# Optimization experiments

Hardware: AMD Instinct MI355X
Metric: run time of the kernel (lower is better)

The kernel has to match this reference:

```python
import jax, jax.numpy as jnp
import numpy as np

N_CLASS = 50257
EMB = 1024
HID = 1024
BATCH = 1024  # must equal HID due to the module's [H,H] zero state init
SEQ = 128


def setup_inputs() -> dict:
    key = jax.random.key(0)
    ks = jax.random.split(key, 8)
    s_e = 1.0 / np.sqrt(EMB)
    s_h = 1.0 / np.sqrt(HID)
    X = jax.random.randint(ks[0], (BATCH, SEQ), 0, N_CLASS, dtype=jnp.int32)
    C = jax.random.normal(ks[1], (N_CLASS, EMB), dtype=jnp.float32)
    # gate order along last axis: i, f, g, o (each block of size HID)
    Wx = jax.random.uniform(ks[2], (EMB, 4 * HID), jnp.float32, -s_e, s_e)
    bx = jax.random.uniform(ks[3], (4 * HID,), jnp.float32, -s_e, s_e)
    Wh = jax.random.uniform(ks[4], (HID, 4 * HID), jnp.float32, -s_h, s_h)
    bh = jax.random.uniform(ks[5], (4 * HID,), jnp.float32, -s_h, s_h)
    W_out = jax.random.uniform(ks[6], (HID, N_CLASS), jnp.float32, -s_h, s_h)
    b_out = jnp.ones((N_CLASS,), dtype=jnp.float32)  # nn.Parameter(torch.ones)
    return {"X": X, "C": C, "Wx": Wx, "bx": bx, "Wh": Wh, "bh": bh,
            "W_out": W_out, "b_out": b_out}


def _lstm_last_hidden(xs, Wx, bx, Wh, bh):
    # xs: [S, B, E]; with zero-initialized h/c of shape [H,H] and B == H,
    # the original broadcast-buggy code reduces to a standard LSTM.
    x_proj = jnp.einsum('sbe,eg->sbg', xs, Wx) + bx  # [S, B, 4H]
    B = xs.shape[1]
    H = Wh.shape[0]
    h0 = jnp.zeros((B, H), dtype=xs.dtype)
    c0 = jnp.zeros((B, H), dtype=xs.dtype)

    def step(carry, xp):
        h, c = carry
        gates = xp + h @ Wh + bh  # [B, 4H]
        i, f, g, o = jnp.split(gates, 4, axis=-1)
        i = jax.nn.sigmoid(i)
        f = jax.nn.sigmoid(f)
        g = jnp.tanh(g)
        o = jax.nn.sigmoid(o)
        c = f * c + i * g
        h = o * jnp.tanh(c)
        return (h, c), None

    (h, _), _ = jax.lax.scan(step, (h0, c0), x_proj)
    return h  # [B, H] last timestep hidden


def reference(X, C, Wx, bx, Wh, bh, W_out, b_out):
    emb = C[X]                      # [B, S, E]
    xs = jnp.swapaxes(emb, 0, 1)    # [S, B, E]  (transpose(0,1))
    h_last = _lstm_last_hidden(xs, Wx, bx, Wh, bh)
    return h_last @ W_out + b_out   # [B, n_class]
```

## Files before the change

### kernel.cpp

```cpp
#include <hip/hip_runtime.h>
#include <hip/hip_bf16.h>

#define SEQ_   128
#define NCLS_  50257
#define EMB_   1024
#define HID_   1024
#define BATCH_ 1024
#define G4_    4096

typedef __attribute__((ext_vector_type(8))) short short8;
typedef __attribute__((ext_vector_type(4))) float f32x4;

__device__ __forceinline__ void async_copy16(void* lds, const void* g) {
  __builtin_amdgcn_global_load_lds(
      (const __attribute__((address_space(1))) void*)g,
      (__attribute__((address_space(3))) void*)lds, 16, 0, 0);
}

#define MFMA_ACC(c, a, b) \
  (c) = __builtin_amdgcn_mfma_f32_16x16x32_bf16((a), (b), (c), 0, 0, 0)

#define CFENCE() asm volatile("" ::: "memory")

__device__ __forceinline__ float sigmoidf_(float x) {
  return 1.f / (1.f + __expf(-x));
}
__device__ __forceinline__ float tanhf_(float x) {
  x = fminf(12.f, fmaxf(-12.f, x));
  float e = __expf(2.f * x);
  return (e - 1.f) / (e + 1.f);
}
__device__ __forceinline__ float bf2f_(ushort u) {
  return __uint_as_float(((unsigned int)u) << 16);
}

template <int EPI>
__global__ __launch_bounds__(256) void gemm_bt(
    const __hip_bfloat16* __restrict__ A, const __hip_bfloat16* __restrict__ Bt,
    float* __restrict__ outF, __hip_bfloat16* __restrict__ outB,
    int Mreal, int Nreal, int K, long ostride,
    const float* __restrict__ bias0) {
  __shared__ __align__(16) char smem[65536];

  const int tid = threadIdx.x;
  const int lane = tid & 63;
  const int w = tid >> 6;
  const int wm = w >> 1;
  const int wn = w & 1;
  const int m0 = blockIdx.y * 128;
  const int n0 = blockIdx.x * 128;

  const int fr = lane & 15;
  const int kb = (lane >> 4) * 16;
  const int swz = (fr & 7) << 4;

  f32x4 acc[4][4];
#pragma unroll
  for (int i = 0; i < 4; ++i)
#pragma unroll
    for (int j = 0; j < 4; ++j) acc[i][j] = (f32x4)(0.0f);

  auto STAGE = [&](int kc, int b) {
#pragma unroll
    for (int q = 0; q < 8; ++q) {
      const int ridx = (q & 3) * 256 + tid;
      const int row = ridx >> 3;
      const int ch = ridx & 7;
      const __hip_bfloat16* src;
      char* dst;
      if (q < 4) {
        long ar = m0 + row; if (ar >= Mreal) ar = Mreal - 1;
        src = A + ar * (long)K + kc * 64 + ch * 8;
        dst = smem + b * 16384 + ridx * 16;
      } else {
        long br = n0 + row; if (br >= Nreal) br = Nreal - 1;
        src = Bt + br * (long)K + kc * 64 + ch * 8;
        dst = smem + 32768 + b * 16384 + ridx * 16;
      }
      async_copy16(dst, src);
    }
  };

  const int KC = K >> 6;
  STAGE(0, 0);
  for (int kc = 0; kc < KC; ++kc) {
    const int b = kc & 1;
    if (kc + 1 < KC) {
      STAGE(kc + 1, b ^ 1);
      asm volatile("s_waitcnt vmcnt(8)" ::: "memory");
    } else {
      asm volatile("s_waitcnt vmcnt(0)" ::: "memory");
    }
    __builtin_amdgcn_s_barrier();
    CFENCE();

    short8 aR[2][4], bR[2][4];
#pragma unroll
    for (int kk = 0; kk < 2; ++kk)
#pragma unroll
      for (int f = 0; f < 4; ++f) {
        aR[kk][f] = *(const short8*)(smem + b * 16384 +
                     (wm * 64 + f * 16 + fr) * 128 + ((kk * 64 + kb) ^ swz));
        bR[kk][f] = *(const short8*)(smem + 32768 + b * 16384 +
                     (wn * 64 + f * 16 + fr) * 128 + ((kk * 64 + kb) ^ swz));
      }
#pragma unroll
    for (int fm = 0; fm < 4; ++fm)
#pragma unroll
      for (int fn = 0; fn < 4; ++fn) {
        MFMA_ACC(acc[fm][fn], aR[0][fm], bR[0][fn]);
        MFMA_ACC(acc[fm][fn], aR[1][fm], bR[1][fn]);
      }
    CFENCE();
    __builtin_amdgcn_s_barrier();
  }

  const int cn = lane & 15;
  const int rb = (lane >> 4) * 4;

  if (EPI == 0) {
    __hip_bfloat16* ldsC = (__hip_bfloat16*)smem;
#pragma unroll
    for (int fn = 0; fn < 4; ++fn) {
      const int col = wn * 64 + fn * 16 + cn;
      const float badd = bias0[n0 + col];
#pragma unroll
      for (int fm = 0; fm < 4; ++fm)
#pragma unroll
        for (int r = 0; r < 4; ++r)
          ldsC[(wm * 64 + fm * 16 + rb + r) * 136 + col] =
              __float2bfloat16(acc[fm][fn][r] + badd);
    }
    __syncthreads();
#pragma unroll
    for (int q = 0; q < 8; ++q) {
      const int chunk = q * 256 + tid;
      const int row = chunk >> 4;
      const int c8 = (chunk & 15) * 8;
      if (m0 + row < Mreal)
        *(short8*)(outB + (long)(m0 + row) * ostride + n0 + c8) =
            *(const short8*)(ldsC + row * 136 + c8);
    }
  } else {
    float* ldsC = (float*)smem;
#pragma unroll
    for (int half = 0; half < 2; ++half) {
      __syncthreads();
      if (wm == half) {
#pragma unroll
        for (int fn = 0; fn < 4; ++fn) {
          const int col = wn * 64 + fn * 16 + cn;
          const int gc = n0 + col;
          const float badd = (gc < Nreal) ? bias0[gc] : 0.f;
#pragma unroll
          for (int fm = 0; fm < 4; ++fm)
#pragma unroll
            for (int r = 0; r < 4; ++r)
              ldsC[(fm * 16 + rb + r) * 132 + col] = acc[fm][fn][r] + badd;
        }
      }
      __syncthreads();
#pragma unroll
      for (int it = 0; it < 32; ++it) {
        const int idx = it * 256 + tid;
        const int row = idx >> 7;
        const int col = idx & 127;
        const int grow = m0 + half * 64 + row;
        const int gcol = n0 + col;
        if (grow < Mreal && gcol < Nreal)
          outF[(long)grow * ostride + gcol] = ldsC[row * 132 + col];
      }
    }
  }
}

__global__ __launch_bounds__(256) void pack_b(const float* __restrict__ Wh,
                                              __hip_bfloat16* __restrict__ Bpk) {
  const int gtid = blockIdx.x * 256 + threadIdx.x;
  const int l = gtid & 63;
  const int tile = gtid >> 6;
  const int g = tile & 3;
  const int kk = (tile >> 2) & 1;
  const int kc = (tile >> 3) & 7;
  const int kh = (tile >> 6) & 1;
  const int wn = (tile >> 7) & 1;
  const int ht = tile >> 8;
  const int h = ht * 32 + wn * 16 + (l & 15);
  const int k0 = kh * 512 + kc * 64 + kk * 32 + (l >> 4) * 8;
  short8 v;
#pragma unroll
  for (int e = 0; e < 8; ++e) {
    const __hip_bfloat16 b = __float2bfloat16(Wh[(size_t)(k0 + e) * G4_ + g * 1024 + h]);
    v[e] = *reinterpret_cast<const short*>(&b);
  }
  *(short8*)(Bpk + (size_t)gtid * 8) = v;
}

__global__ __launch_bounds__(512, 2) void lstm_step(
    const __hip_bfloat16* __restrict__ hprev,
    const __hip_bfloat16* __restrict__ Bpk,
    const __hip_bfloat16* __restrict__ Epr,
    const int* __restrict__ X,
    float* __restrict__ cbuf,
    __hip_bfloat16* __restrict__ hnext,
    int t) {
  extern __shared__ __align__(16) char smem[];
  float* gacc = (float*)smem;

  const int tid = threadIdx.x;
  const int lane = tid & 63;
  const int w = tid >> 6;
  const int wm = (w >> 1) & 1;
  const int wn = w & 1;
  const int kh = w >> 2;
  const int bid = blockIdx.x;
  const int xcd = bid & 7;
  const int j = bid >> 3;
  const int ht = xcd * 4 + (j & 3);
  const int mt = j >> 2;
  const int m0 = mt * 128;
  const int h0 = ht * 32;

  const int fr = lane & 15;
  const int kb = (lane >> 4) * 16;
  const int swz = (fr & 7) << 4;
  const int cn = lane & 15;
  const int rb = (lane >> 4) * 4;

  const int crow = tid >> 2;
  const int hq = tid & 3;
  const int prow = m0 + crow;
  const int tok1 = X[prow * SEQ_ + t];

  const __hip_bfloat16* bb =
      Bpk + (size_t)(((ht * 2 + wn) * 2 + kh) * 64) * 512 + lane * 8;

  ushort4 ep[8];
  float cold[8];
#pragma unroll
  for (int jj = 0; jj < 8; ++jj) {
    ep[jj] = *(const ushort4*)(Epr + (size_t)tok1 * G4_ + (h0 + hq * 8 + jj) * 4);
    cold[jj] = cbuf[(size_t)prow * HID_ + h0 + hq * 8 + jj];
  }
  CFENCE();

  f32x4 acc[4][4];
#pragma unroll
  for (int i = 0; i < 4; ++i)
#pragma unroll
    for (int g = 0; g < 4; ++g) acc[i][g] = (f32x4)(0.0f);

  auto STAGE_A = [&](int kc, int b) {
#pragma unroll
    for (int q = 0; q < 4; ++q) {
      const int region = q >> 1;
      const int r = (q & 1) * 512 + tid;
      const int row = r >> 3, ch = r & 7;
      const __hip_bfloat16* src =
          hprev + (size_t)(m0 + row) * HID_ + region * 512 + kc * 64 + ch * 8;
      async_copy16(smem + b * 32768 + region * 16384 + r * 16, src);
    }
  };

  short8 bR[2][2][4];

  STAGE_A(0, 0);
#pragma unroll
  for (int kk = 0; kk < 2; ++kk)
#pragma unroll
    for (int g = 0; g < 4; ++g)
      bR[0][kk][g] = *(const short8*)(bb + (0 * 8 + kk * 4 + g) * 512);
  STAGE_A(1, 1);

#pragma unroll
  for (int kc = 0; kc < 8; ++kc) {
    __builtin_amdgcn_s_barrier();
    CFENCE();
    if (kc + 1 < 8) {
#pragma unroll
      for (int kk = 0; kk < 2; ++kk)
#pragma unroll
        for (int g = 0; g < 4; ++g)
          bR[(kc + 1) & 1][kk][g] =
              *(const short8*)(bb + ((kc + 1) * 8 + kk * 4 + g) * 512);
    }
    if (kc + 2 < 8) STAGE_A(kc + 2, (kc + 2) % 3);
    if (kc < 6)      asm volatile("s_waitcnt vmcnt(24)" ::: "memory");
    else if (kc == 6) asm volatile("s_waitcnt vmcnt(20)" ::: "memory");
    else             asm volatile("s_waitcnt vmcnt(8)" ::: "memory");
    CFENCE();

    const char* baseA = smem + (kc % 3) * 32768 + kh * 16384;
    short8 aR[2][4];
#pragma unroll
    for (int kk = 0; kk < 2; ++kk)
#pragma unroll
      for (int f = 0; f < 4; ++f)
        aR[kk][f] = *(const short8*)(baseA + (wm * 64 + f * 16 + fr) * 128 +
                                     ((kk * 64 + kb) ^ swz));
    __builtin_amdgcn_s_setprio(1);
#pragma unroll
    for (int fm = 0; fm < 4; ++fm)
#pragma unroll
      for (int g = 0; g < 4; ++g) {
        MFMA_ACC(acc[fm][g], aR[0][fm], bR[kc & 1][0][g]);
        MFMA_ACC(acc[fm][g], aR[1][fm], bR[kc & 1][1][g]);
      }
    __builtin_amdgcn_s_setprio(0);
    CFENCE();
  }

  __syncthreads();
  if (kh == 0) {
#pragma unroll
    for (int fm = 0; fm < 4; ++fm)
#pragma unroll
      for (int g = 0; g < 4; ++g)
#pragma unroll
        for (int r = 0; r < 4; ++r)
          gacc[(wm * 64 + fm * 16 + rb + r) * 132 + (wn * 16 + cn) * 4 + g] =
              acc[fm][g][r];
  }
  __syncthreads();
  if (kh == 1) {
#pragma unroll
    for (int fm = 0; fm < 4; ++fm)
#pragma unroll
      for (int g = 0; g < 4; ++g)
#pragma unroll
        for (int r = 0; r < 4; ++r)
          gacc[(wm * 64 + fm * 16 + rb + r) * 132 + (wn * 16 + cn) * 4 + g] +=
              acc[fm][g][r];
  }
  __syncthreads();

  const float* gr = gacc + crow * 132 + hq * 32;
  f32x4 cnew0, cnew1;
  short8 hv;
#pragma unroll
  for (int jj = 0; jj < 8; ++jj) {
    const f32x4 g4 = *(const f32x4*)(gr + jj * 4);
    const float iv = sigmoidf_(g4[0] + bf2f_(ep[jj].x));
    const float fv = sigmoidf_(g4[1] + bf2f_(ep[jj].y));
    const float gv = tanhf_(g4[2] + bf2f_(ep[jj].z));
    const float ov = sigmoidf_(g4[3] + bf2f_(ep[jj].w));
    const float cv = fv * cold[jj] + iv * gv;
    if (jj < 4) cnew0[jj] = cv; else cnew1[jj - 4] = cv;
    const float hval = ov * tanhf_(cv);
    const __hip_bfloat16 hb = __float2bfloat16(hval);
    hv[jj] = *reinterpret_cast<const short*>(&hb);
  }
  float* cdst = cbuf + (size_t)prow * HID_ + h0 + hq * 8;
  *(f32x4*)cdst = cnew0;
  *(f32x4*)(cdst + 4) = cnew1;
  const int hcolb = h0 + hq * 8;
  const int hswb = (hcolb & ~63) | ((hcolb & 63) ^ ((prow & 7) << 3));
  *(short8*)(hnext + (size_t)prow * HID_ + hswb) = hv;
}

template <bool SWZ>
__global__ __launch_bounds__(256) void conv_bf16_k(const float* __restrict__ in,
                                                   __hip_bfloat16* __restrict__ out, int n4) {
  const int i = blockIdx.x * 256 + threadIdx.x;
  if (i >= n4) return;
  const float4 v = ((const float4*)in)[i];
  int o = i * 4;
  if (SWZ) {
    const int row = o >> 10, col = o & 1023;
    const int cs = (col & ~63) | ((col & 63) ^ ((row & 7) << 3));
    o = (o & ~1023) | cs;
  }
  out[o + 0] = __float2bfloat16(v.x);
  out[o + 1] = __float2bfloat16(v.y);
  out[o + 2] = __float2bfloat16(v.z);
  out[o + 3] = __float2bfloat16(v.w);
}

template <bool PERM, bool SWZ>
__global__ __launch_bounds__(256) void transpose_conv(const float* __restrict__ in,
                                                      __hip_bfloat16* __restrict__ out,
                                                      int R, int C) {
  __shared__ float tile[32][33];
  const int c0 = blockIdx.x * 32, r0 = blockIdx.y * 32;
  const int tx = threadIdx.x, ty = threadIdx.y;
#pragma unroll
  for (int i = 0; i < 4; ++i) {
    const int r = r0 + ty + i * 8, cc = c0 + tx;
    tile[ty + i * 8][tx] = (r < R && cc < C) ? in[(size_t)r * C + cc] : 0.f;
  }
  __syncthreads();
#pragma unroll
  for (int i = 0; i < 4; ++i) {
    const int ro = c0 + ty + i * 8, co = r0 + tx;
    if (ro < C && co < R) {
      const int n = PERM ? ((ro & 1023) * 4 + (ro >> 10)) : ro;
      int k = co;
      if (SWZ) k = (k & ~63) | ((k & 63) ^ ((n & 7) << 3));
      out[(size_t)n * R + k] = __float2bfloat16(tile[tx][ty + i * 8]);
    }
  }
}

__global__ __launch_bounds__(256) void bias_perm(const float* __restrict__ bx,
                                                 const float* __restrict__ bh,
                                                 float* __restrict__ bP) {
  const int n = blockIdx.x * 256 + threadIdx.x;
  if (n >= G4_) return;
  const int h = n >> 2, g = n & 3;
  bP[n] = bx[g * HID_ + h] + bh[g * HID_ + h];
}

extern "C" void kernel_launch(void* const* d_in, const int* in_sizes, int n_in,
                              void* d_out, int out_size, void* d_ws, size_t ws_size,
                              hipStream_t stream) {
  const int* X = (const int*)d_in[0];
  const float* C = (const float*)d_in[1];
  const float* Wx = (const float*)d_in[2];
  const float* bx = (const float*)d_in[3];
  const float* Wh = (const float*)d_in[4];
  const float* bh = (const float*)d_in[5];
  const float* Wo = (const float*)d_in[6];
  const float* bo = (const float*)d_in[7];
  float* out = (float*)d_out;

  char* p = (char*)d_ws;
  const size_t szCb  = (size_t)NCLS_ * EMB_ * 2;
  const size_t szWxt = (size_t)G4_ * EMB_ * 2;
  const size_t szBpk = (size_t)G4_ * HID_ * 2;
  const size_t szEpr = (size_t)NCLS_ * G4_ * 2;
  const size_t szH   = (size_t)BATCH_ * HID_ * 2;
  const size_t szC   = (size_t)BATCH_ * HID_ * 4;
  const size_t szBp  = (size_t)G4_ * 4;
  if (ws_size < szCb + szWxt + szBpk + szEpr + 2 * szH + szC + szBp) return;

  __hip_bfloat16* Cb   = (__hip_bfloat16*)p; p += szCb;
  __hip_bfloat16* WxtP = (__hip_bfloat16*)p; p += szWxt;
  __hip_bfloat16* Bpk  = (__hip_bfloat16*)p; p += szBpk;
  __hip_bfloat16* Epr  = (__hip_bfloat16*)p; p += szEpr;
  __hip_bfloat16* hA   = (__hip_bfloat16*)p; p += szH;
  __hip_bfloat16* hB   = (__hip_bfloat16*)p; p += szH;
  float* cbuf          = (float*)p;          p += szC;
  float* bP            = (float*)p;          p += szBp;

  {
    const int n4 = NCLS_ * EMB_ / 4;
    conv_bf16_k<true><<<(n4 + 255) / 256, 256, 0, stream>>>(C, Cb, n4);
  }
  transpose_conv<true, true><<<dim3(G4_ / 32, EMB_ / 32), dim3(32, 8), 0, stream>>>(
      Wx, WxtP, EMB_, G4_);
  pack_b<<<2048, 256, 0, stream>>>(Wh, Bpk);
  bias_perm<<<G4_ / 256, 256, 0, stream>>>(bx, bh, bP);

  gemm_bt<0><<<dim3(G4_ / 128, (NCLS_ + 127) / 128), 256, 0, stream>>>(
      Cb, WxtP, nullptr, Epr, NCLS_, G4_, EMB_, G4_, bP);

  hipMemsetAsync(hA, 0, szH, stream);
  hipMemsetAsync(cbuf, 0, szC, stream);

  for (int t = 0; t < SEQ_; ++t) {
    const __hip_bfloat16* hp = (t & 1) ? hB : hA;
    __hip_bfloat16* hn = (t & 1) ? hA : hB;
    lstm_step<<<256, 512, 98304, stream>>>(hp, Bpk, Epr, X, cbuf, hn, t);
  }

  __hip_bfloat16* Wot = Cb;
  transpose_conv<false, true><<<dim3((NCLS_ + 31) / 32, HID_ / 32), dim3(32, 8), 0,
                                stream>>>(Wo, Wot, HID_, NCLS_);

  gemm_bt<2><<<dim3((NCLS_ + 127) / 128, BATCH_ / 128), 256, 0, stream>>>(
      hA, Wot, out, nullptr, BATCH_, NCLS_, HID_, NCLS_, bo);
}
```

Measured before the change: 3.018 ms.

## Use 256x256-tile GEMM for embedding projection and defer per-step epilogue loads

Replaces the 128x128 bf16 GEMM that precomputes the embedding-table projection (50257x4096x1024) with a dedicated 512-thread, 256x256-tile kernel that uses 128KB of double-buffered LDS. Each block does more MFMA work per staged byte. It also moves the Epr and cell-state loads in the LSTM step kernel from before the K-loop to after it, which lowers register pressure during the MFMA loop but exposes their latency at the end. The larger tiles lower occupancy and waste more work on the ragged final row tile.

```diff
diff --git a/kernel.cpp b/kernel.cpp
--- a/kernel.cpp
+++ b/kernel.cpp
@@ -34,11 +34,123 @@
   return __uint_as_float(((unsigned int)u) << 16);
 }
 
-template <int EPI>
-__global__ __launch_bounds__(256) void gemm_bt(
+__global__ __launch_bounds__(512) void gemm256e(
+    const __hip_bfloat16* __restrict__ A,
+    const __hip_bfloat16* __restrict__ Bt,
+    __hip_bfloat16* __restrict__ outB,
+    int Mreal, int Nreal, const float* __restrict__ bias0) {
+  extern __shared__ __align__(16) char smem[];
+
+  const int tid = threadIdx.x;
+  const int lane = tid & 63;
+  const int w = tid >> 6;
+  const int wm = w >> 2;
+  const int wn = w & 3;
+  const int m0 = blockIdx.y * 256;
+  const int n0 = blockIdx.x * 256;
+
+  const int fr = lane & 15;
+  const int kb = (lane >> 4) * 16;
+  const int swz = (fr & 7) << 4;
+
+  f32x4 acc[8][4];
+#pragma unroll
+  for (int i = 0; i < 8; ++i)
+#pragma unroll
+    for (int j = 0; j < 4; ++j) acc[i][j] = (f32x4)(0.0f);
+
+  auto STAGE = [&](int kc, int b) {
+#pragma unroll
+    for (int q = 0; q < 8; ++q) {
+      const int r = (q & 3) * 512 + tid;
+      const int row = r >> 3;
+      const int ch = r & 7;
+      const __hip_bfloat16* src;
+      char* dst;
+      if (q < 4) {
+        long ar = m0 + row; if (ar >= Mreal) ar = Mreal - 1;
+        src = A + ar * 1024 + kc * 64 + ch * 8;
+        dst = smem + b * 65536 + r * 16;
+      } else {
+        long br = n0 + row; if (br >= Nreal) br = Nreal - 1;
+        src = Bt + br * 1024 + kc * 64 + ch * 8;
+        dst = smem + b * 65536 + 32768 + r * 16;
+      }
+      async_copy16(dst, src);
+    }
+  };
+
+  STAGE(0, 0);
+  for (int kc = 0; kc < 16; ++kc) {
+    const int b = kc & 1;
+    if (kc + 1 < 16) {
+      STAGE(kc + 1, b ^ 1);
+      asm volatile("s_waitcnt vmcnt(8)" ::: "memory");
+    } else {
+      asm volatile("s_waitcnt vmcnt(0)" ::: "memory");
+    }
+    __builtin_amdgcn_s_barrier();
+    CFENCE();
+
+#pragma unroll
+    for (int kk = 0; kk < 2; ++kk) {
+      short8 aR[8], bR[4];
+#pragma unroll
+      for (int f = 0; f < 8; ++f)
+        aR[f] = *(const short8*)(smem + b * 65536 +
+                 (wm * 128 + f * 16 + fr) * 128 + ((kk * 64 + kb) ^ swz));
+#pragma unroll
+      for (int f = 0; f < 4; ++f)
+        bR[f] = *(const short8*)(smem + b * 65536 + 32768 +
+                 (wn * 64 + f * 16 + fr) * 128 + ((kk * 64 + kb) ^ swz));
+      __builtin_amdgcn_s_setprio(1);
+#pragma unroll
+      for (int fm = 0; fm < 8; ++fm)
+#pragma unroll
+        for (int fn = 0; fn < 4; ++fn)
+          MFMA_ACC(acc[fm][fn], aR[fm], bR[fn]);
+      __builtin_amdgcn_s_setprio(0);
+    }
+    CFENCE();
+    __builtin_amdgcn_s_barrier();
+  }
+
+  const int cn = lane & 15;
+  const int rb = (lane >> 4) * 4;
+  __hip_bfloat16* ldsC = (__hip_bfloat16*)smem;
+#pragma unroll
+  for (int half = 0; half < 2; ++half) {
+    __syncthreads();
+    if (wm == half) {
+#pragma unroll
+      for (int fn = 0; fn < 4; ++fn) {
+        const int col = wn * 64 + fn * 16 + cn;
+        const float badd = bias0[n0 + col];
+#pragma unroll
+        for (int fm = 0; fm < 8; ++fm)
+#pragma unroll
+          for (int r = 0; r < 4; ++r)
+            ldsC[(fm * 16 + rb + r) * 264 + col] =
+                __float2bfloat16(acc[fm][fn][r] + badd);
+      }
+    }
+    __syncthreads();
+#pragma unroll
+    for (int q = 0; q < 8; ++q) {
+      const int chunk = q * 512 + tid;
+      const int row = chunk >> 5;
+      const int c8 = (chunk & 31) * 8;
+      const int grow = m0 + half * 128 + row;
+      if (grow < Mreal)
+        *(short8*)(outB + (long)grow * G4_ + n0 + c8) =
+            *(const short8*)(ldsC + row * 264 + c8);
+    }
+  }
+}
+
+__global__ __launch_bounds__(256) void gemm_bt2(
     const __hip_bfloat16* __restrict__ A, const __hip_bfloat16* __restrict__ Bt,
-    float* __restrict__ outF, __hip_bfloat16* __restrict__ outB,
-    int Mreal, int Nreal, int K, long ostride,
+    float* __restrict__ outF, int Mreal, int Nreal, int K, long ostride,
     const float* __restrict__ bias0) {
   __shared__ __align__(16) char smem[65536];
 
@@ -117,59 +229,33 @@
 
   const int cn = lane & 15;
   const int rb = (lane >> 4) * 4;
-
-  if (EPI == 0) {
-    __hip_bfloat16* ldsC = (__hip_bfloat16*)smem;
-#pragma unroll
-    for (int fn = 0; fn < 4; ++fn) {
-      const int col = wn * 64 + fn * 16 + cn;
-      const float badd = bias0[n0 + col];
-#pragma unroll
-      for (int fm = 0; fm < 4; ++fm)
-#pragma unroll
-        for (int r = 0; r < 4; ++r)
-          ldsC[(wm * 64 + fm * 16 + rb + r) * 136 + col] =
-              __float2bfloat16(acc[fm][fn][r] + badd);
-    }
+  float* ldsC = (float*)smem;
+#pragma unroll
+  for (int half = 0; half < 2; ++half) {
     __syncthreads();
-#pragma unroll
-    for (int q = 0; q < 8; ++q) {
-      const int chunk = q * 256 + tid;
-      const int row = chunk >> 4;
-      const int c8 = (chunk & 15) * 8;
-      if (m0 + row < Mreal)
-        *(short8*)(outB + (long)(m0 + row) * ostride + n0 + c8) =
-            *(const short8*)(ldsC + row * 136 + c8);
-    }
-  } else {
-    float* ldsC = (float*)smem;
-#pragma unroll
-    for (int half = 0; half < 2; ++half) {
-      __syncthreads();
-      if (wm == half) {
-#pragma unroll
-        for (int fn = 0; fn < 4; ++fn) {
-          const int col = wn * 64 + fn * 16 + cn;
-          const int gc = n0 + col;
-          const float badd = (gc < Nreal) ? bias0[gc] : 0.f;
-#pragma unroll
-          for (int fm = 0; fm < 4; ++fm)
-#pragma unroll
-            for (int r = 0; r < 4; ++r)
-              ldsC[(fm * 16 + rb + r) * 132 + col] = acc[fm][fn][r] + badd;
-        }
-      }
-      __syncthreads();
-#pragma unroll
-      for (int it = 0; it < 32; ++it) {
-        const int idx = it * 256 + tid;
-        const int row = idx >> 7;
-        const int col = idx & 127;
-        const int grow = m0 + half * 64 + row;
-        const int gcol = n0 + col;
-        if (grow < Mreal && gcol < Nreal)
-          outF[(long)grow * ostride + gcol] = ldsC[row * 132 + col];
-      }
+    if (wm == half) {
+#pragma unroll
+      for (int fn = 0; fn < 4; ++fn) {
+        const int col = wn * 64 + fn * 16 + cn;
+        const int gc = n0 + col;
+        const float badd = (gc < Nreal) ? bias0[gc] : 0.f;
+#pragma unroll
+        for (int fm = 0; fm < 4; ++fm)
+#pragma unroll
+          for (int r = 0; r < 4; ++r)
+            ldsC[(fm * 16 + rb + r) * 132 + col] = acc[fm][fn][r] + badd;
+      }
+    }
+    __syncthreads();
+#pragma unroll
+    for (int it = 0; it < 32; ++it) {
+      const int idx = it * 256 + tid;
+      const int row = idx >> 7;
+      const int col = idx & 127;
+      const int grow = m0 + half * 64 + row;
+      const int gcol = n0 + col;
+      if (grow < Mreal && gcol < Nreal)
+        outF[(long)grow * ostride + gcol] = ldsC[row * 132 + col];
     }
   }
 }
@@ -235,15 +321,6 @@
   const __hip_bfloat16* bb =
       Bpk + (size_t)(((ht * 2 + wn) * 2 + kh) * 64) * 512 + lane * 8;
 
-  ushort4 ep[8];
-  float cold[8];
-#pragma unroll
-  for (int jj = 0; jj < 8; ++jj) {
-    ep[jj] = *(const ushort4*)(Epr + (size_t)tok1 * G4_ + (h0 + hq * 8 + jj) * 4);
-    cold[jj] = cbuf[(size_t)prow * HID_ + h0 + hq * 8 + jj];
-  }
-  CFENCE();
-
   f32x4 acc[4][4];
 #pragma unroll
   for (int i = 0; i < 4; ++i)
@@ -308,6 +385,14 @@
       }
     __builtin_amdgcn_s_setprio(0);
     CFENCE();
+  }
+
+  ushort4 ep[8];
+  float cold[8];
+#pragma unroll
+  for (int jj = 0; jj < 8; ++jj) {
+    ep[jj] = *(const ushort4*)(Epr + (size_t)tok1 * G4_ + (h0 + hq * 8 + jj) * 4);
+    cold[jj] = cbuf[(size_t)prow * HID_ + h0 + hq * 8 + jj];
   }
 
   __syncthreads();
@@ -451,8 +536,8 @@
   pack_b<<<2048, 256, 0, stream>>>(Wh, Bpk);
   bias_perm<<<G4_ / 256, 256, 0, stream>>>(bx, bh, bP);
 
-  gemm_bt<0><<<dim3(G4_ / 128, (NCLS_ + 127) / 128), 256, 0, stream>>>(
-      Cb, WxtP, nullptr, Epr, NCLS_, G4_, EMB_, G4_, bP);
+  gemm256e<<<dim3(G4_ / 256, (NCLS_ + 255) / 256), 512, 131072, stream>>>(
+      Cb, WxtP, Epr, NCLS_, G4_, bP);
 
   hipMemsetAsync(hA, 0, szH, stream);
   hipMemsetAsync(cbuf, 0, szC, stream);
@@ -467,6 +552,6 @@
   transpose_conv<false, true><<<dim3((NCLS_ + 31) / 32, HID_ / 32), dim3(32, 8), 0,
                                 stream>>>(Wo, Wot, HID_, NCLS_);
 
-  gemm_bt<2><<<dim3((NCLS_ + 127) / 128, BATCH_ / 128), 256, 0, stream>>>(
-      hA, Wot, out, nullptr, BATCH_, NCLS_, HID_, NCLS_, bo);
-}
+  gemm_bt2<<<dim3((NCLS_ + 127) / 128, BATCH_ / 128), 256, 0, stream>>>(
+      hA, Wot, out, BATCH_, NCLS_, HID_, NCLS_, bo);
+}
```

After: 2.942 ms. 2.5% less time.
